# Performance work log

Hardware: AMD Instinct MI355X
Metric: run time of the kernel (lower is better)

The kernel has to match this reference:

```python
import jax, jax.numpy as jnp
import numpy as np
from math import factorial

N_SCALES = 4
K_ORI = 4
NA = 9


def _grids(h, w):
    fy = (jnp.arange(h) - h // 2) * (2.0 / h)
    fx = (jnp.arange(w) - w // 2) * (2.0 / w)
    FY, FX = jnp.meshgrid(fy, fx, indexing='ij')
    r = jnp.sqrt(FX ** 2 + FY ** 2)
    r = jnp.where(r == 0, 1.0 / max(h, w), r)
    return jnp.log2(r), jnp.arctan2(FY, FX)


def _rc_hi(lr, lo, hi):
    # sqrt raised-cosine rising 0->1 over log_rad in [lo, hi]
    t = jnp.clip((lr - lo) / (hi - lo), 0.0, 1.0)
    return jnp.sqrt(0.5 * (1.0 - jnp.cos(jnp.pi * t)))


def _rc_lo(lr, lo, hi):
    t = jnp.clip((lr - lo) / (hi - lo), 0.0, 1.0)
    return jnp.sqrt(0.5 * (1.0 + jnp.cos(jnp.pi * t)))


def _angle_masks(angle, K, is_complex):
    order = K - 1
    const = (2.0 ** (2 * order)) * (factorial(order) ** 2) / (K * factorial(2 * order))
    masks = []
    for b in range(K):
        d = jnp.mod(angle - jnp.pi * b / K + jnp.pi, 2 * jnp.pi) - jnp.pi
        if is_complex:  # single-sided (analytic) mask
            m = 2.0 * np.sqrt(const) * (jnp.cos(d) ** order) * (jnp.abs(d) < jnp.pi / 2)
        else:
            m = np.sqrt(const) * (jnp.cos(d) ** order)
        masks.append(m)
    return masks


def _build_pyramid(img, n_scales, K):
    # complex steerable pyramid in the frequency domain (tight_frame=False)
    order = K - 1
    h, w = img.shape
    imdft = jnp.fft.fftshift(jnp.fft.fft2(img))
    lr, ang = _grids(h, w)
    hi0 = _rc_hi(lr, -1.0, 0.0)
    lo0 = _rc_lo(lr, -1.0, 0.0)
    coeffs = {'residual_highpass': jnp.real(jnp.fft.ifft2(jnp.fft.ifftshift(imdft * hi0)))}
    lodft = imdft * lo0
    cph = (-1j) ** order
    for s in range(n_scales):
        hh, ww = lodft.shape
        lr, ang = _grids(hh, ww)
        him = _rc_hi(lr, -2.0, -1.0)
        for b, am in enumerate(_angle_masks(ang, K, True)):
            coeffs[(s, b)] = jnp.fft.ifft2(jnp.fft.ifftshift(cph * lodft * him * am))
        # spectral crop = spatial downsample by 2, then lowpass
        lodft = lodft[hh // 4: hh // 4 + hh // 2, ww // 4: ww // 4 + ww // 2]
        lr2, _ = _grids(hh // 2, ww // 2)
        lodft = lodft * _rc_lo(lr2, -1.0, 0.0)
    coeffs['residual_lowpass'] = jnp.real(jnp.fft.ifft2(jnp.fft.ifftshift(lodft)))
    return coeffs


def _lo0_filter(im):
    # height-0 pyramid residual lowpass == lo0 filtering (filterPyr in the torch code)
    h, w = im.shape
    lr, _ = _grids(h, w)
    return jnp.real(jnp.fft.ifft2(jnp.fft.ifftshift(jnp.fft.fftshift(jnp.fft.fft2(im)) * _rc_lo(lr, -1.0, 0.0))))


def _expand(im, f=2):
    # frequency-domain upsampling by factor f (Portilla_Simoncelli.expand)
    h, w = im.shape
    dft = jnp.fft.fftshift(jnp.fft.fft2(im)).astype(jnp.complex64)
    big = jnp.zeros((f * h, f * w), dtype=jnp.complex64)
    big = big.at[(f * h - h) // 2:(f * h - h) // 2 + h, (f * w - w) // 2:(f * w - w) // 2 + w].set(dft)
    return jnp.fft.ifft2(jnp.fft.ifftshift(big)) * (f * f)


def _recon_band(real_bands, K):
    # recon_pyr(levels=[0]) of a height-1 real pyramid whose bands were replaced
    order = K - 1
    h, w = real_bands[0].shape
    lr, ang = _grids(h, w)
    lo0 = _rc_lo(lr, -1.0, 0.0)
    him = _rc_hi(lr, -2.0, -1.0)
    ph = (1j) ** order
    recondft = jnp.zeros((h, w), dtype=jnp.complex64)
    for b, am in enumerate(_angle_masks(ang, K, False)):
        recondft = recondft + ph * jnp.fft.fftshift(jnp.fft.fft2(real_bands[b])) * him * am
    return jnp.real(jnp.fft.ifft2(jnp.fft.ifftshift(recondft * lo0)))


def _autocorr(ch, la):
    h, w = ch.shape
    F = jnp.fft.fft2(ch)
    ac = jnp.fft.fftshift(jnp.real(jnp.fft.ifft2(jnp.abs(F) ** 2))) / (h * w)
    cx, cy = h // 2, w // 2
    le = int(min(min(h, w) / 2 - 1, la))
    return ac[cx - le:cx + le + 1, cy - le:cy + le + 1], ac[cx, cy], le


def _skew_kurt(ch, vari, var0):
    cond = (vari / var0) > 1e-6
    skew = jnp.where(cond, jnp.mean(ch ** 3) / (vari ** 1.5), 0.0)
    kurt = jnp.where(cond, jnp.mean(ch ** 4) / (vari ** 2), 3.0)
    return skew, kurt


def _ps_forward(image):
    n_scales, K, Na = N_SCALES, K_ORI, NA
    img = image.reshape(image.shape[-2], image.shape[-1])
    mu = jnp.mean(img)
    var0 = jnp.var(img, ddof=1)
    cimg = img - mu
    pix = jnp.stack([mu, var0,
                     jnp.mean(cimg ** 3) / (var0 ** 1.5),
                     jnp.mean(cimg ** 4) / (var0 ** 2),
                     jnp.min(img), jnp.max(img)])
    coeffs = _build_pyramid(img, n_scales, K)
    coeffs['residual_lowpass'] = coeffs['residual_lowpass'] - jnp.mean(coeffs['residual_lowpass'])
    keys = ['residual_highpass'] + [(s, b) for s in range(n_scales) for b in range(K)] + ['residual_lowpass']
    mag, realc, mag_means = {}, {}, []
    for kk in keys:
        v = coeffs[kk]
        m = jnp.abs(v)
        mm = jnp.mean(m)
        mag_means.append(mm)
        mag[kk] = m - mm
        realc[kk] = jnp.real(v)
    mag_means = jnp.stack(mag_means)
    la = (Na - 1) // 2
    auto_corr = jnp.zeros((Na, Na, n_scales + 1))
    acm = jnp.zeros((Na, Na, n_scales, K))
    skew_r = jnp.zeros((n_scales + 1,))
    kurt_r = jnp.zeros((n_scales + 1,))
    recon = _lo0_filter(coeffs['residual_lowpass'])
    patch, vari, le = _autocorr(recon, la)
    auto_corr = auto_corr.at[la - le:la + le + 1, la - le:la + le + 1, n_scales].set(patch)
    sk, ku = _skew_kurt(recon, vari, var0)
    skew_r = skew_r.at[n_scales].set(sk)
    kurt_r = kurt_r.at[n_scales].set(ku)
    for s in range(n_scales - 1, -1, -1):
        for b in range(K):
            patch, vari, le = _autocorr(mag[(s, b)], la)
            acm = acm.at[la - le:la + le + 1, la - le:la + le + 1, s, b].set(patch)
        recon = jnp.real(_expand(recon, 2) / 4.0)
        recon = recon + _recon_band([realc[(s, b)] for b in range(K)], K)
        patch, vari, le = _autocorr(recon, la)
        auto_corr = auto_corr.at[la - le:la + le + 1, la - le:la + le + 1, s].set(patch)
        sk, ku = _skew_kurt(recon, vari, var0)
        skew_r = skew_r.at[s].set(sk)
        kurt_r = kurt_r.at[s].set(ku)
    K2 = max(2 * K, 5)
    coc_mag = jnp.zeros((K, K, n_scales + 1))
    csc_mag = jnp.zeros((K, K, n_scales))
    coc_real = jnp.zeros((K2, K2, n_scales + 1))
    csc_real = jnp.zeros((2 * K, K2, n_scales))
    for s in range(n_scales):
        hs, ws = realc[(s, 0)].shape
        csz = hs * ws
        if s < n_scales - 1:
            pars, rpr, rpi = [], [], []
            for b in range(K):
                tmp = _expand(coeffs[(s + 1, b)], 2) / 4.0
                rt, it = jnp.real(tmp), jnp.imag(tmp)
                mg = jnp.sqrt(rt ** 2 + it ** 2)
                a2 = 2.0 * jnp.arctan2(rt, it)  # note arg order matches torch code
                rpr.append((mg * jnp.cos(a2)).T.reshape(-1))
                rpi.append((mg * jnp.sin(a2)).T.reshape(-1))
                pars.append((mg - jnp.mean(mg)).T.reshape(-1))
            parents = jnp.stack(pars, 1)
            rparents = jnp.stack(rpr + rpi, 1)
        else:
            tmp = jnp.real(_expand(coeffs['residual_lowpass'], 2) / 4.0).T
            rparents = jnp.stack([tmp.reshape(-1),
                                  jnp.roll(tmp, 1, 0).reshape(-1),
                                  jnp.roll(tmp, -1, 0).reshape(-1),
                                  jnp.roll(tmp, 1, 1).reshape(-1),
                                  jnp.roll(tmp, -1, 1).reshape(-1)], 1)
            parents = None
        cousins = jnp.stack([mag[(s, b)].T.reshape(-1) for b in range(K)], 1)
        coc_mag = coc_mag.at[:, :, s].set(cousins.T @ cousins / csz)
        if parents is not None:
            csc_mag = csc_mag.at[:, :, s].set(cousins.T @ parents / csz)
        rcousins = jnp.stack([realc[(s, b)].T.reshape(-1) for b in range(K)], 1)
        coc_real = coc_real.at[:K, :K, s].set(rcousins.T @ rcousins / csz)
        nrp = rparents.shape[1]
        csc_real = csc_real.at[:K, :nrp, s].set(rcousins.T @ rparents / csz)
        if s == n_scales - 1:
            coc_real = coc_real.at[:nrp, :nrp, n_scales].set(rparents.T @ rparents / (csz / 4.0))
    var_hp = jnp.mean(coeffs['residual_highpass'] ** 2)
    return jnp.concatenate([pix, mag_means, acm.reshape(-1), skew_r, kurt_r,
                            auto_corr.reshape(-1), coc_mag.reshape(-1), csc_mag.reshape(-1),
                            coc_real.reshape(-1), csc_real.reshape(-1), var_hp.reshape(1)])


def setup_inputs() -> dict:
    key = jax.random.key(0)
    image = jax.random.normal(key, (1, 1, 1024, 1024), dtype=jnp.float32)
    return {"image": image}


def reference(image):
    return _ps_forward(image)
```

## Files before the change

### kernel.cpp

```cpp
#include <hip/hip_runtime.h>
#include <math.h>

typedef float2 cplx;

#define PI_F 3.14159265358979323846f
#define SQC  0.8944271909999159f

#define GS_FOR(i, n) for (int i = blockIdx.x * blockDim.x + threadIdx.x; i < (n); i += gridDim.x * blockDim.x)
#define RED_GRID 256

#define MD_PLAIN 0
#define MD_R2C   1
#define MD_HP    2
#define MD_BAND  3
#define MD_EMB   4

__device__ __forceinline__ float ufreq(int i, int n) {
  return (float)((i < (n >> 1)) ? i : i - n) * (2.0f / (float)n);
}
__device__ __forceinline__ void grid_lr_ang(int i, int j, int n, float* lr, float* ang) {
  float fy = ufreq(i, n), fx = ufreq(j, n);
  float r = sqrtf(fx * fx + fy * fy);
  if (i == 0 && j == 0) r = 1.0f / (float)n;
  *lr = log2f(r);
  *ang = atan2f(fy, fx);
}
__device__ __forceinline__ float rc_hi_f(float lr, float lo, float hi) {
  float t = (lr - lo) / (hi - lo);
  t = fminf(fmaxf(t, 0.0f), 1.0f);
  return sqrtf(0.5f * (1.0f - cosf(PI_F * t)));
}
__device__ __forceinline__ float rc_lo_f(float lr, float lo, float hi) {
  float t = (lr - lo) / (hi - lo);
  t = fminf(fmaxf(t, 0.0f), 1.0f);
  return sqrtf(0.5f * (1.0f + cosf(PI_F * t)));
}
__device__ __forceinline__ float wrap_d(float ang, int b) {
  float d = ang - PI_F * (float)b * 0.25f + PI_F;
  d = d - floorf(d * (0.5f / PI_F)) * (2.0f * PI_F);
  return d - PI_F;
}
__device__ __forceinline__ float amask_c(float ang, int b) {
  float d = wrap_d(ang, b);
  float c = cosf(d);
  float m = 2.0f * SQC * c * c * c;
  return (fabsf(d) < 0.5f * PI_F) ? m : 0.0f;
}
__device__ __forceinline__ float amask_r(float ang, int b) {
  float d = wrap_d(ang, b);
  float c = cosf(d);
  return SQC * c * c * c;
}

__device__ __forceinline__ double wred_d(double v) {
#pragma unroll
  for (int o = 32; o > 0; o >>= 1) v += __shfl_down(v, o);
  return v;
}
template<int NS>
__device__ __forceinline__ void block_to_parts(double* __restrict__ part, int slotBase, double* v) {
  __shared__ double lds[NS][4];
  const int wid = threadIdx.x >> 6, lane = threadIdx.x & 63;
#pragma unroll
  for (int q = 0; q < NS; ++q) {
    double r = wred_d(v[q]);
    if (lane == 0) lds[q][wid] = r;
  }
  __syncthreads();
  for (int q = threadIdx.x; q < NS; q += blockDim.x) {
    double s = lds[q][0] + lds[q][1] + lds[q][2] + lds[q][3];
    part[(size_t)(slotBase + q) * RED_GRID + blockIdx.x] = s;
  }
}
__global__ void reduce_parts_k(double* __restrict__ acc, const double* __restrict__ part, int base) {
  const double* p = part + (size_t)(base + blockIdx.x) * RED_GRID;
  double s = 0;
  for (int i = threadIdx.x; i < RED_GRID; i += 64) s += p[i];
  s = wred_d(s);
  if (threadIdx.x == 0) acc[base + blockIdx.x] = s;
}
__device__ __forceinline__ void atomicMinF(float* a, float v) {
  if (v >= 0.0f) atomicMin((int*)a, __float_as_int(v));
  else atomicMax((unsigned int*)a, __float_as_uint(v));
}
__device__ __forceinline__ void atomicMaxF(float* a, float v) {
  if (v >= 0.0f) atomicMax((int*)a, __float_as_int(v));
  else atomicMin((unsigned int*)a, __float_as_uint(v));
}

template<int LOGN, bool INV, int MODE>
__global__ __launch_bounds__(256) void fftm_k(cplx* __restrict__ dst, const void* __restrict__ srcv,
                                              const cplx* __restrict__ aux, int b0) {
  constexpr int N = 1 << LOGN;
  __shared__ cplx sh[N];
  __shared__ cplx tw[N / 2];
  const int tid = threadIdx.x;
  const int T = blockDim.x;
  const int r = blockIdx.x;
  const int i = r & (N - 1);
  const int p = r >> LOGN;
  for (int k = tid; k < N / 2; k += T) {
    float a = (INV ? 2.0f : -2.0f) * PI_F * (float)k / (float)N;
    float s, c;
    sincosf(a, &s, &c);
    tw[k] = make_float2(c, s);
  }
  for (int j = tid; j < N; j += T) {
    cplx v;
    if (MODE == MD_PLAIN) {
      v = ((const cplx*)srcv)[(size_t)r * N + j];
    } else if (MODE == MD_R2C) {
      v = make_float2(((const float*)srcv)[(size_t)r * N + j], 0.0f);
    } else if (MODE == MD_HP) {
      v = ((const cplx*)srcv)[(size_t)r * N + j];
      float lr, ang;
      grid_lr_ang(i, j, N, &lr, &ang);
      float h0 = rc_hi_f(lr, -1.0f, 0.0f);
      v.x *= h0; v.y *= h0;
    } else if (MODE == MD_BAND) {
      float lr, ang;
      grid_lr_ang(i, j, N, &lr, &ang);
      float m = rc_hi_f(lr, -2.0f, -1.0f) * amask_c(ang, b0 + p);
      cplx z = aux[i * N + j];
      v = make_float2(-z.y * m, z.x * m);
    } else {
      const int Nc = N >> 1, q = Nc >> 1;
      int ci = (i < q) ? i : ((i >= N - q) ? (i - N + Nc) : -1);
      int cj = (j < q) ? j : ((j >= N - q) ? (j - N + Nc) : -1);
      v = make_float2(0.0f, 0.0f);
      if (ci >= 0 && cj >= 0) {
        float lr, ang;
        grid_lr_ang(ci, cj, Nc, &lr, &ang);
        float m = rc_hi_f(lr, -2.0f, -1.0f) * amask_c(ang, b0 + p);
        cplx z = aux[ci * Nc + cj];
        v = make_float2(-z.y * m, z.x * m);
      }
    }
    unsigned rr = __brev((unsigned)j) >> (32 - LOGN);
    sh[rr] = v;
  }
  __syncthreads();
  for (int len = 2; len <= N; len <<= 1) {
    const int half = len >> 1;
    const int tstep = N / len;
    for (int j = tid; j < N / 2; j += T) {
      int pos = j & (half - 1);
      int base = (j - pos) << 1;
      cplx w = tw[pos * tstep];
      cplx a = sh[base + pos];
      cplx b = sh[base + pos + half];
      float tx = b.x * w.x - b.y * w.y;
      float ty = b.x * w.y + b.y * w.x;
      sh[base + pos] = make_float2(a.x + tx, a.y + ty);
      sh[base + pos + half] = make_float2(a.x - tx, a.y - ty);
    }
    __syncthreads();
  }
  const float sc = INV ? (1.0f / (float)N) : 1.0f;
  for (int j = tid; j < N; j += T) {
    cplx v = sh[j];
    dst[(size_t)r * N + j] = make_float2(v.x * sc, v.y * sc);
  }
}

__global__ void transpose_k(cplx* __restrict__ out, const cplx* __restrict__ in, int N) {
  __shared__ cplx tile[32][33];
  size_t po = (size_t)blockIdx.z * N * N;
  int bx = blockIdx.x * 32, by = blockIdx.y * 32;
  int x = bx + threadIdx.x;
  for (int dy = threadIdx.y; dy < 32; dy += 8)
    tile[dy][threadIdx.x] = in[po + (size_t)(by + dy) * N + x];
  __syncthreads();
  int xo = by + threadIdx.x;
  for (int dy = threadIdx.y; dy < 32; dy += 8)
    out[po + (size_t)(bx + dy) * N + xo] = tile[threadIdx.x][dy];
}

__global__ void lod_only_k(cplx* lod, const cplx* spec, int logN) {
  int N = 1 << logN, n = N * N;
  GS_FOR(idx, n) {
    int i = idx >> logN, j = idx & (N - 1);
    float lr, ang;
    grid_lr_ang(i, j, N, &lr, &ang);
    float l0 = rc_lo_f(lr, -1.0f, 0.0f);
    cplx z = spec[idx];
    lod[idx] = make_float2(z.x * l0, z.y * l0);
  }
}
__global__ void rhp_stats_k(const cplx* src, int n, double* part) {
  double sa = 0, sq = 0;
  GS_FOR(i, n) {
    float v = src[i].x;
    sa += fabsf(v);
    sq += (double)v * (double)v;
  }
  double v[2] = {sa, sq};
  block_to_parts<2>(part, 4, v);
}
template<int P>
__global__ void extract_band_k(float* realc, float* mag, const cplx* src, int logPer,
                               double* part, int slotBase) {
  int n = (1 << logPer) * P;
  double s0 = 0, s1 = 0, s2 = 0, s3 = 0;
  GS_FOR(idx, n) {
    cplx z = src[idx];
    float m = sqrtf(z.x * z.x + z.y * z.y);
    realc[idx] = z.x;
    mag[idx] = m;
    int p = idx >> logPer;
    if (p == 0) s0 += m; else if (p == 1) s1 += m; else if (p == 2) s2 += m; else s3 += m;
  }
  double v[4] = {s0, s1, s2, s3};
  block_to_parts<P>(part, slotBase, v);
}
__global__ void center_k(float* buf, int logPer, int P, const double* acc0) {
  int nPer = 1 << logPer, n = nPer * P;
  double inv = 1.0 / (double)nPer;
  GS_FOR(idx, n) buf[idx] -= (float)(acc0[idx >> logPer] * inv);
}
__global__ void lod_down_k(cplx* child, const cplx* par, int logNc) {
  int Nc = 1 << logNc, n = Nc * Nc, Np = Nc << 1;
  GS_FOR(idx, n) {
    int i = idx >> logNc, j = idx & (Nc - 1);
    int pi = (i < (Nc >> 1)) ? i : i + Nc;
    int pj = (j < (Nc >> 1)) ? j : j + Nc;
    float lr, ang;
    grid_lr_ang(i, j, Nc, &lr, &ang);
    float l0 = rc_lo_f(lr, -1.0f, 0.0f);
    cplx z = par[pi * Np + pj];
    child[idx] = make_float2(z.x * l0, z.y * l0);
  }
}
__global__ void sum_real2_k(const cplx* src, int n, double* part) {
  double s = 0;
  GS_FOR(i, n) s += (double)src[i].x;
  double v[1] = {s};
  block_to_parts<1>(part, 24, v);
}
__global__ void center_abs2_k(const cplx* src, int n, const double* acc, double* part) {
  float mu = (float)(acc[24] / (double)n);
  double s = 0;
  GS_FOR(i, n) s += fabsf(src[i].x - mu);
  double v[1] = {s};
  block_to_parts<1>(part, 25, v);
}
__global__ void rs4_init_k(cplx* rs, const cplx* lod4) {
  GS_FOR(idx, 4096) {
    int i = idx >> 6, j = idx & 63;
    float lr, ang;
    grid_lr_ang(i, j, 64, &lr, &ang);
    float l0 = rc_lo_f(lr, -1.0f, 0.0f);
    cplx v = lod4[idx];
    if (idx == 0) v = make_float2(0.0f, 0.0f);
    rs[idx] = make_float2(v.x * l0, v.y * l0);
  }
}
__global__ void embed_rs_k(cplx* dst, const cplx* src, int logNb, int zeroDC) {
  int Nb = 1 << logNb, Nc = Nb >> 1, q = Nc >> 1, n = Nb * Nb;
  GS_FOR(idx, n) {
    int i = idx >> logNb, j = idx & (Nb - 1);
    int ci = (i < q) ? i : ((i >= Nb - q) ? (i - Nb + Nc) : -1);
    int cj = (j < q) ? j : ((j >= Nb - q) ? (j - Nb + Nc) : -1);
    cplx v = make_float2(0.0f, 0.0f);
    if (ci >= 0 && cj >= 0) {
      v = src[ci * Nc + cj];
      if (zeroDC && ci == 0 && cj == 0) v = make_float2(0.0f, 0.0f);
    }
    dst[idx] = v;
  }
}
__global__ void recon_step_k(cplx* __restrict__ dst, const cplx* __restrict__ src,
                             const cplx* __restrict__ lod, int logNb) {
  int Nb = 1 << logNb, Nc = Nb >> 1, qq = Nc >> 1, n = Nb * Nb;
  GS_FOR(idx, n) {
    int i = idx >> logNb, j = idx & (Nb - 1);
    int ci = (i < qq) ? i : ((i >= Nb - qq) ? (i - Nb + Nc) : -1);
    int cj = (j < qq) ? j : ((j >= Nb - qq) ? (j - Nb + Nc) : -1);
    float ex = 0.0f, ey = 0.0f;
    if (ci >= 0 && cj >= 0) { cplx v = src[ci * Nc + cj]; ex = v.x; ey = v.y; }
    int ni = (Nb - i) & (Nb - 1), nj = (Nb - j) & (Nb - 1);
    float lr, ang;
    grid_lr_ang(i, j, Nb, &lr, &ang);
    float him = rc_hi_f(lr, -2.0f, -1.0f);
    float l0 = rc_lo_f(lr, -1.0f, 0.0f);
    cplx L = lod[idx];
    cplx L2 = lod[ni * Nb + nj];
    float sx = 0.0f, sy = 0.0f;
#pragma unroll
    for (int b = 0; b < 4; ++b) {
      float c1 = him * amask_c(ang, b);
      float c2 = him * amask_c(ang + PI_F, b);
      float mr = him * amask_r(ang, b);
      float gx = L.x * c1 - L2.x * c2;
      float gy = L.y * c1 + L2.y * c2;
      sx += 0.5f * mr * gx;
      sy += 0.5f * mr * gy;
    }
    dst[idx] = make_float2(ex + sx * l0, ey + sy * l0);
  }
}
template<int ST, bool SK>
__device__ __forceinline__ void ac_core(const float* __restrict__ xp, int logN,
                                        double* __restrict__ part, int slotBase) {
  const int N = 1 << logN;
  const int nu = (N * N) >> 3;
  float acc[41];
#pragma unroll
  for (int q = 0; q < 41; ++q) acc[q] = 0.0f;
  float a3 = 0.0f, a4 = 0.0f;
  for (int u = blockIdx.x * blockDim.x + threadIdx.x; u < nu; u += gridDim.x * blockDim.x) {
    int i = u >> (logN - 3);
    int j0 = (u & ((N >> 3) - 1)) << 3;
    float buf[5][16];
#pragma unroll
    for (int di = 0; di < 5; ++di) {
      int r = ((i + di) & (N - 1)) << logN;
#pragma unroll
      for (int blk = 0; blk < 4; ++blk) {
        int c = (j0 - 4 + blk * 4) & (N - 1);
        if (ST == 1) {
          const float4 v = *reinterpret_cast<const float4*>(xp + r + c);
          buf[di][blk * 4 + 0] = v.x; buf[di][blk * 4 + 1] = v.y;
          buf[di][blk * 4 + 2] = v.z; buf[di][blk * 4 + 3] = v.w;
        } else {
          const float4 v0 = *reinterpret_cast<const float4*>(xp + ((size_t)(r + c) << 1));
          const float4 v1 = *reinterpret_cast<const float4*>(xp + ((size_t)(r + c) << 1) + 4);
          buf[di][blk * 4 + 0] = v0.x; buf[di][blk * 4 + 1] = v0.z;
          buf[di][blk * 4 + 2] = v1.x; buf[di][blk * 4 + 3] = v1.z;
        }
      }
    }
#pragma unroll
    for (int k = 0; k < 8; ++k) {
      float xc = buf[0][4 + k];
      if (SK) {
        float x2 = xc * xc;
        a3 += x2 * xc;
        a4 += x2 * x2;
      }
#pragma unroll
      for (int q = 0; q < 41; ++q) {
        const int di = (q < 5) ? 0 : 1 + (q - 5) / 9;
        const int dj = (q < 5) ? q : ((q - 5) % 9) - 4;
        acc[q] += xc * buf[di][4 + k + dj];
      }
    }
  }
  constexpr int NS = SK ? 43 : 41;
  double v[NS];
#pragma unroll
  for (int q = 0; q < 41; ++q) v[q] = (double)acc[q];
  if (SK) { v[41] = (double)a3; v[42] = (double)a4; }
  block_to_parts<NS>(part, slotBase, v);
}
__global__ __launch_bounds__(256) void acm_vec_k(const float* m0, const float* m1,
                                                 const float* m2, const float* m3, double* part) {
  const int s = blockIdx.z;
  const float* base = (s == 0) ? m0 : ((s == 1) ? m1 : ((s == 2) ? m2 : m3));
  const int logN = 10 - s;
  const float* xp = base + ((size_t)blockIdx.y << (2 * logN));
  ac_core<1, false>(xp, logN, part, 448 + (s * 4 + blockIdx.y) * 41);
}
__global__ __launch_bounds__(256) void ac_rec_k(const float* x, int logN, double* part, int slotBase) {
  ac_core<2, true>(x, logN, part, slotBase);
}
__global__ void img_stats1_k(const float* img, int n, double* part, float* mm) {
  double s = 0;
  float mn = INFINITY, mx = -INFINITY;
  GS_FOR(i, n) {
    float v = img[i];
    s += (double)v;
    mn = fminf(mn, v);
    mx = fmaxf(mx, v);
  }
  double v[1] = {s};
  block_to_parts<1>(part, 0, v);
#pragma unroll
  for (int o = 32; o > 0; o >>= 1) {
    mn = fminf(mn, __shfl_down(mn, o));
    mx = fmaxf(mx, __shfl_down(mx, o));
  }
  if ((threadIdx.x & 63) == 0) {
    atomicMinF(mm + 0, mn);
    atomicMaxF(mm + 1, mx);
  }
}
__global__ void img_stats2_k(const float* img, int n, const double* acc, double* part) {
  double mu = acc[0] / (double)n;
  double s2 = 0, s3 = 0, s4 = 0;
  GS_FOR(i, n) {
    double c = (double)img[i] - mu;
    double c2 = c * c;
    s2 += c2;
    s3 += c2 * c;
    s4 += c2 * c2;
  }
  double v[3] = {s2, s3, s4};
  block_to_parts<3>(part, 1, v);
}
template<bool WS>
__global__ void gram4_k(const float* base, int n, double* part, int slotBase) {
  constexpr int NS = WS ? 20 : 16;
  double g[16];
  double s[4];
#pragma unroll
  for (int q = 0; q < 16; ++q) g[q] = 0;
#pragma unroll
  for (int q = 0; q < 4; ++q) s[q] = 0;
  GS_FOR(i, n) {
    double d0 = base[i], d1 = base[n + i], d2 = base[2 * n + i], d3 = base[3 * n + i];
    g[0] += d0 * d0; g[1] += d0 * d1; g[2]  += d0 * d2; g[3]  += d0 * d3;
    g[5] += d1 * d1; g[6] += d1 * d2; g[7]  += d1 * d3;
    g[10] += d2 * d2; g[11] += d2 * d3;
    g[15] += d3 * d3;
    if (WS) { s[0] += d0; s[1] += d1; s[2] += d2; s[3] += d3; }
  }
  g[4] = g[1]; g[8] = g[2]; g[12] = g[3]; g[9] = g[6]; g[13] = g[7]; g[14] = g[11];
  double v[NS];
#pragma unroll
  for (int q = 0; q < 16; ++q) v[q] = g[q];
  if (WS) {
#pragma unroll
    for (int q = 0; q < 4; ++q) v[16 + q] = s[q];
  }
  block_to_parts<NS>(part, slotBase, v);
}
__global__ void parent_reduce_k(const cplx* par, const float* magS, const float* realS, int n,
                                double* part, int slotBase) {
  double d[13];
#pragma unroll
  for (int q = 0; q < 13; ++q) d[q] = 0;
  GS_FOR(i, n) {
    cplx z = par[i];
    float rt = z.x, it = z.y;
    float mg = sqrtf(rt * rt + it * it);
    float rpr = 0.0f, rpi = 0.0f;
    if (mg > 0.0f) {
      rpr = (it * it - rt * rt) / mg;
      rpi = 2.0f * rt * it / mg;
    }
    d[0] += (double)mg;
#pragma unroll
    for (int b = 0; b < 4; ++b) d[1 + b] += (double)magS[b * n + i] * (double)mg;
#pragma unroll
    for (int b = 0; b < 4; ++b) {
      double rv = (double)realS[b * n + i];
      d[5 + b] += rv * (double)rpr;
      d[9 + b] += rv * (double)rpi;
    }
  }
  block_to_parts<13>(part, slotBase, d);
}
__global__ void lp_parent2_k(const cplx* X, const float* realS, int logN, double* part) {
  int N = 1 << logN, n = N * N;
  double d[45];
#pragma unroll
  for (int q = 0; q < 45; ++q) d[q] = 0;
  GS_FOR(idx, n) {
    int i = idx >> logN, j = idx & (N - 1);
    float c[5];
    c[0] = X[idx].x;
    c[1] = X[((i - 1) & (N - 1)) * N + j].x;
    c[2] = X[((i + 1) & (N - 1)) * N + j].x;
    c[3] = X[i * N + ((j - 1) & (N - 1))].x;
    c[4] = X[i * N + ((j + 1) & (N - 1))].x;
#pragma unroll
    for (int b = 0; b < 4; ++b) {
      double rv = (double)realS[b * n + idx];
#pragma unroll
      for (int k = 0; k < 5; ++k) d[b * 5 + k] += rv * (double)c[k];
    }
#pragma unroll
    for (int a = 0; a < 5; ++a)
#pragma unroll
      for (int k = 0; k < 5; ++k) d[20 + a * 5 + k] += (double)c[a] * (double)c[k];
  }
  block_to_parts<45>(part, 370, d);
}
__global__ void init_mm_k(float* mm) {
  if (threadIdx.x == 0) { mm[0] = INFINITY; mm[1] = -INFINITY; }
}

__global__ void assemble_k(float* out, const double* acc, const float* mm) {
  const int t = threadIdx.x;
  const double NPIX = 1048576.0;
  double var0 = acc[1] / (NPIX - 1.0);
  if (t == 0) {
    double mu = acc[0] / NPIX;
    out[0] = (float)mu;
    out[1] = (float)var0;
    out[2] = (float)((acc[2] / NPIX) / pow(var0, 1.5));
    out[3] = (float)((acc[3] / NPIX) / (var0 * var0));
    out[4] = mm[0];
    out[5] = mm[1];
    out[2455] = (float)(acc[5] / NPIX);
  }
  for (int k = t; k < 18; k += blockDim.x) {
    double n, sv;
    if (k == 0) { n = NPIX; sv = acc[4]; }
    else if (k == 17) { n = 4096.0; sv = acc[25]; }
    else { int s = (k - 1) >> 2; double dd = (double)(1024 >> s); n = dd * dd; sv = acc[7 + k]; }
    out[6 + k] = (float)(sv / n);
  }
  for (int si = t; si < 5; si += blockDim.x) {
    double dd = (si == 4) ? 64.0 : (double)(1024 >> si);
    double nn = dd * dd;
    double vari = acc[1104 + si * 43] / nn;
    bool cond = (vari / var0) > 1e-6;
    double m3 = acc[1104 + si * 43 + 41] / nn, m4 = acc[1104 + si * 43 + 42] / nn;
    out[1320 + si] = (float)(cond ? m3 / pow(vari, 1.5) : 0.0);
    out[1325 + si] = (float)(cond ? m4 / (vari * vari) : 3.0);
  }
  for (int w = t; w < 656; w += blockDim.x) {
    int patch = w / 41, q = w - patch * 41;
    int s = patch >> 2, b = patch & 3;
    double dd = (double)(1024 >> s);
    double v = acc[448 + w] / (dd * dd);
    int di = (q < 5) ? 0 : 1 + (q - 5) / 9;
    int dj = (q < 5) ? q : ((q - 5) % 9) - 4;
    int pi = 4 + dj, pj = 4 + di;
    out[24 + 144 * pi + 16 * pj + 4 * s + b] = (float)v;
    if (q) out[24 + 144 * (8 - pi) + 16 * (8 - pj) + 4 * s + b] = (float)v;
  }
  for (int w = t; w < 205; w += blockDim.x) {
    int si = w / 41, q = w - si * 41;
    double dd = (si == 4) ? 64.0 : (double)(1024 >> si);
    double v = acc[1104 + si * 43 + q] / (dd * dd);
    int di = (q < 5) ? 0 : 1 + (q - 5) / 9;
    int dj = (q < 5) ? q : ((q - 5) % 9) - 4;
    int pi = 4 + dj, pj = 4 + di;
    out[1330 + (pi * 9 + pj) * 5 + si] = (float)v;
    if (q) out[1330 + ((8 - pi) * 9 + (8 - pj)) * 5 + si] = (float)v;
  }
  for (int q = t; q < 64; q += blockDim.x) {
    int s = q >> 4, ij = q & 15;
    double dd = (double)(1024 >> s); double csz = dd * dd;
    out[1735 + ij * 5 + s] = (float)(acc[64 + s * 20 + ij] / csz);
  }
  for (int q = t; q < 64; q += blockDim.x) {
    int s = q >> 4, ij = q & 15;
    int i = ij >> 2, j = ij & 3;
    double dd = (double)(1024 >> s); double csz = dd * dd;
    out[1879 + (i * 8 + j) * 5 + s] = (float)(acc[144 + s * 16 + ij] / csz);
  }
  for (int q = t; q < 25; q += blockDim.x) {
    int a = q / 5, b2 = q - a * 5;
    out[1879 + (a * 8 + b2) * 5 + 4] = (float)(acc[390 + q] / 4096.0);
  }
  for (int q = t; q < 48; q += blockDim.x) {
    int s = q >> 4, ij = q & 15;
    int i = ij >> 2, pb = ij & 3;
    double dd = (double)(1024 >> s); double csz = dd * dd;
    const double* ps = acc + 208 + (s * 4 + pb) * 13;
    double meanp = ps[0] / csz;
    double cousSum = acc[64 + s * 20 + 16 + i];
    out[1815 + (i * 4 + pb) * 4 + s] = (float)((ps[1 + i] - meanp * cousSum) / csz);
  }
  for (int q = t; q < 96; q += blockDim.x) {
    int s = q >> 5, r = q & 31;
    int i = r >> 3, j = r & 7;
    int pb = j & 3, offq = (j >= 4) ? 9 : 5;
    double dd = (double)(1024 >> s); double csz = dd * dd;
    out[2199 + (i * 8 + j) * 4 + s] = (float)(acc[208 + (s * 4 + pb) * 13 + offq + i] / csz);
  }
  for (int q = t; q < 20; q += blockDim.x) {
    int i = q / 5, c = q - i * 5;
    out[2199 + (i * 8 + c) * 4 + 3] = (float)(acc[370 + q] / 16384.0);
  }
}

static inline int thr_for(int N) { return (N >= 512) ? 256 : ((N == 256) ? 128 : 64); }
template<int MODE>
static void fft_pass(int N, int rows, bool inv, cplx* dst, const void* src, const cplx* aux,
                     int b0, hipStream_t st) {
  dim3 g(rows), b(thr_for(N));
  switch (N) {
    case 64:
      if (inv) fftm_k<6, true, MODE><<<g, b, 0, st>>>(dst, src, aux, b0);
      else     fftm_k<6, false, MODE><<<g, b, 0, st>>>(dst, src, aux, b0);
      break;
    case 128:
      if (inv) fftm_k<7, true, MODE><<<g, b, 0, st>>>(dst, src, aux, b0);
      else     fftm_k<7, false, MODE><<<g, b, 0, st>>>(dst, src, aux, b0);
      break;
    case 256:
      if (inv) fftm_k<8, true, MODE><<<g, b, 0, st>>>(dst, src, aux, b0);
      else     fftm_k<8, false, MODE><<<g, b, 0, st>>>(dst, src, aux, b0);
      break;
    case 512:
      if (inv) fftm_k<9, true, MODE><<<g, b, 0, st>>>(dst, src, aux, b0);
      else     fftm_k<9, false, MODE><<<g, b, 0, st>>>(dst, src, aux, b0);
      break;
    case 1024:
      if (inv) fftm_k<10, true, MODE><<<g, b, 0, st>>>(dst, src, aux, b0);
      else     fftm_k<10, false, MODE><<<g, b, 0, st>>>(dst, src, aux, b0);
      break;
    default: break;
  }
}
static void transp(cplx* out, const cplx* in, int N, int P, hipStream_t st) {
  dim3 tg(N / 32, N / 32, P), tb(32, 8);
  transpose_k<<<tg, tb, 0, st>>>(out, in, N);
}
template<int MODE>
static void ifft2dT(int N, int P, cplx* out, cplx* tmp, const void* src, const cplx* aux,
                    int b0, hipStream_t st) {
  fft_pass<MODE>(N, N * P, true, tmp, src, aux, b0, st);
  transp(out, tmp, N, P, st);
  fft_pass<MD_PLAIN>(N, N * P, true, out, out, nullptr, 0, st);
}
static inline dim3 gsz(int n) {
  int b = (n + 255) >> 8;
  if (b > 2048) b = 2048;
  if (b < 1) b = 1;
  return dim3(b);
}

extern "C" void kernel_launch(void* const* d_in, const int* in_sizes, int n_in,
                              void* d_out, int out_size, void* d_ws, size_t ws_size,
                              hipStream_t stream) {
  (void)in_sizes; (void)n_in; (void)out_size; (void)ws_size;
  const float* img = (const float*)d_in[0];
  float* out = (float*)d_out;

  char* wsb = (char*)d_ws;
  size_t off = 0;
  auto alloc = [&](size_t bytes) -> void* {
    void* p = wsb + off;
    off += (bytes + 255) & ~(size_t)255;
    return p;
  };
  const size_t MB = (size_t)1 << 20;
  const int NSLOT = 1320;
  cplx* cA = (cplx*)alloc(16 * MB);
  cplx* cB = (cplx*)alloc(16 * MB);
  cplx* LOD[5];
  for (int s = 0; s < 5; ++s) {
    int N = 1024 >> s;
    LOD[s] = (cplx*)alloc((size_t)N * N * sizeof(cplx));
  }
  cplx* RS[4];
  for (int k = 0; k < 4; ++k) {
    int N = 64 << k;
    RS[k] = (cplx*)alloc((size_t)N * N * sizeof(cplx));
  }
  float* MAG[4];
  float* REALC[4];
  for (int s = 0; s < 4; ++s) {
    int N = 1024 >> s;
    MAG[s] = (float*)alloc((size_t)4 * N * N * sizeof(float));
  }
  for (int s = 0; s < 4; ++s) {
    int N = 1024 >> s;
    REALC[s] = (float*)alloc((size_t)4 * N * N * sizeof(float));
  }
  const int NPIX = 1024 * 1024;
  double* PART = (double*)alloc((size_t)NSLOT * RED_GRID * 8);
  double* ACC  = (double*)alloc(2048 * 8);
  float* MM    = (float*)alloc(256);

  auto finish = [&](int base, int count) {
    reduce_parts_k<<<dim3(count), 64, 0, stream>>>(ACC, PART, base);
  };

  hipMemsetAsync(out, 0, 2456 * sizeof(float), stream);
  init_mm_k<<<1, 64, 0, stream>>>(MM);

  img_stats1_k<<<dim3(RED_GRID), 256, 0, stream>>>(img, NPIX, PART, MM);
  finish(0, 1);
  img_stats2_k<<<dim3(RED_GRID), 256, 0, stream>>>(img, NPIX, ACC, PART);

  fft_pass<MD_R2C>(1024, 1024, false, cA, img, nullptr, 0, stream);
  transp(cB, cA, 1024, 1, stream);
  fft_pass<MD_PLAIN>(1024, 1024, false, cB, cB, nullptr, 0, stream);
  transp(cA, cB, 1024, 1, stream);
  lod_only_k<<<gsz(NPIX), 256, 0, stream>>>(LOD[0], cA, 10);
  ifft2dT<MD_HP>(1024, 1, cA, cB, cA, nullptr, 0, stream);
  rhp_stats_k<<<dim3(RED_GRID), 256, 0, stream>>>(cA, NPIX, PART);
  for (int b0 = 0; b0 < 4; b0 += 2) {
    ifft2dT<MD_BAND>(1024, 2, cB, cA, nullptr, LOD[0], b0, stream);
    extract_band_k<2><<<dim3(RED_GRID), 256, 0, stream>>>(REALC[0] + (size_t)b0 * NPIX,
                                                          MAG[0] + (size_t)b0 * NPIX, cB, 20, PART, 8 + b0);
  }
  finish(8, 4);
  center_k<<<gsz(4 * NPIX), 256, 0, stream>>>(MAG[0], 20, 4, ACC + 8);
  lod_down_k<<<gsz(512 * 512), 256, 0, stream>>>(LOD[1], LOD[0], 9);
  for (int s = 1; s <= 3; ++s) {
    int N = 1024 >> s, logN = 10 - s, n = N * N;
    ifft2dT<MD_BAND>(N, 4, cB, cA, nullptr, LOD[s], 0, stream);
    extract_band_k<4><<<dim3(RED_GRID), 256, 0, stream>>>(REALC[s], MAG[s], cB, 2 * logN, PART, 8 + 4 * s);
    finish(8 + 4 * s, 4);
    center_k<<<gsz(4 * n), 256, 0, stream>>>(MAG[s], 2 * logN, 4, ACC + 8 + 4 * s);
    lod_down_k<<<gsz((N / 2) * (N / 2)), 256, 0, stream>>>(LOD[s + 1], LOD[s], logN - 1);
  }
  ifft2dT<MD_PLAIN>(64, 1, cB, cA, LOD[4], nullptr, 0, stream);
  sum_real2_k<<<dim3(RED_GRID), 256, 0, stream>>>(cB, 4096, PART);
  finish(24, 1);
  center_abs2_k<<<dim3(RED_GRID), 256, 0, stream>>>(cB, 4096, ACC, PART);

  acm_vec_k<<<dim3(RED_GRID, 4, 4), 256, 0, stream>>>(MAG[0], MAG[1], MAG[2], MAG[3], PART);

  rs4_init_k<<<gsz(4096), 256, 0, stream>>>(RS[0], LOD[4]);
  ifft2dT<MD_PLAIN>(64, 1, cB, cA, RS[0], nullptr, 0, stream);
  ac_rec_k<<<dim3(RED_GRID), 256, 0, stream>>>((const float*)cB, 6, PART, 1104 + 4 * 43);
  cplx* cur = RS[0];
  for (int s = 3; s >= 0; --s) {
    int N = 1024 >> s, logN = 10 - s, n = N * N;
    cplx* sp = (s > 0) ? RS[4 - s] : cB;
    recon_step_k<<<gsz(n), 256, 0, stream>>>(sp, cur, LOD[s], logN);
    ifft2dT<MD_PLAIN>(N, 1, cB, cA, sp, nullptr, 0, stream);
    ac_rec_k<<<dim3(RED_GRID), 256, 0, stream>>>((const float*)cB, logN, PART, 1104 + s * 43);
    cur = sp;
  }

  for (int s = 0; s < 4; ++s) {
    int n = (1024 >> s) * (1024 >> s);
    gram4_k<true><<<dim3(RED_GRID), 256, 0, stream>>>(MAG[s], n, PART, 64 + s * 20);
    gram4_k<false><<<dim3(RED_GRID), 256, 0, stream>>>(REALC[s], n, PART, 144 + s * 16);
  }
  for (int pb0 = 0; pb0 < 4; pb0 += 2) {
    ifft2dT<MD_EMB>(1024, 2, cB, cA, nullptr, LOD[1], pb0, stream);
    for (int p = 0; p < 2; ++p)
      parent_reduce_k<<<dim3(RED_GRID), 256, 0, stream>>>(cB + (size_t)p * NPIX, MAG[0], REALC[0], NPIX,
                                                          PART, 208 + (pb0 + p) * 13);
  }
  for (int s = 1; s <= 2; ++s) {
    int N = 1024 >> s, n = N * N;
    ifft2dT<MD_EMB>(N, 4, cB, cA, nullptr, LOD[s + 1], 0, stream);
    for (int p = 0; p < 4; ++p)
      parent_reduce_k<<<dim3(RED_GRID), 256, 0, stream>>>(cB + (size_t)p * n, MAG[s], REALC[s], n,
                                                          PART, 208 + (s * 4 + p) * 13);
  }
  embed_rs_k<<<gsz(128 * 128), 256, 0, stream>>>(cA, LOD[4], 7, 1);
  ifft2dT<MD_PLAIN>(128, 1, cB, cA + 16384, cA, nullptr, 0, stream);
  lp_parent2_k<<<dim3(RED_GRID), 256, 0, stream>>>(cB, REALC[3], 7, PART);

  finish(0, NSLOT);
  assemble_k<<<1, 256, 0, stream>>>(out, ACC, MM);
}
```

Before: 1.152 ms.

## Replace centering passes with raw-moment corrections and batch reduction launches

Image statistics become a single pass that accumulates raw power sums; skew and kurtosis are then recovered algebraically in the final assembly. The per-scale centering kernels and their finish syncs are dropped, with the mean corrections applied in assembly for the magnitude autocorrelation and covariance. The eight gram launches are merged into one 2D-grid kernel, parent_reduce launches are batched over planes via blockIdx.y, and the reduction grid size is doubled. This cuts full-resolution passes, launches and serialising reductions. The cost is cancellation error from raw-moment formulas, and any consumer of the uncentered magnitudes that lacks a matching correction would produce wrong results.

```diff
diff --git a/kernel.cpp b/kernel.cpp
--- a/kernel.cpp
+++ b/kernel.cpp
@@ -7,7 +7,7 @@
 #define SQC  0.8944271909999159f
 
 #define GS_FOR(i, n) for (int i = blockIdx.x * blockDim.x + threadIdx.x; i < (n); i += gridDim.x * blockDim.x)
-#define RED_GRID 256
+#define RED_GRID 512
 
 #define MD_PLAIN 0
 #define MD_R2C   1
@@ -213,11 +213,6 @@
   double v[4] = {s0, s1, s2, s3};
   block_to_parts<P>(part, slotBase, v);
 }
-__global__ void center_k(float* buf, int logPer, int P, const double* acc0) {
-  int nPer = 1 << logPer, n = nPer * P;
-  double inv = 1.0 / (double)nPer;
-  GS_FOR(idx, n) buf[idx] -= (float)(acc0[idx >> logPer] * inv);
-}
 __global__ void lod_down_k(cplx* child, const cplx* par, int logNc) {
   int Nc = 1 << logNc, n = Nc * Nc, Np = Nc << 1;
   GS_FOR(idx, n) {
@@ -364,17 +359,18 @@
 __global__ __launch_bounds__(256) void ac_rec_k(const float* x, int logN, double* part, int slotBase) {
   ac_core<2, true>(x, logN, part, slotBase);
 }
-__global__ void img_stats1_k(const float* img, int n, double* part, float* mm) {
-  double s = 0;
+__global__ void img_stats_k(const float* img, int n, double* part, float* mm) {
+  double s1 = 0, s2 = 0, s3 = 0, s4 = 0;
   float mn = INFINITY, mx = -INFINITY;
   GS_FOR(i, n) {
-    float v = img[i];
-    s += (double)v;
-    mn = fminf(mn, v);
-    mx = fmaxf(mx, v);
-  }
-  double v[1] = {s};
-  block_to_parts<1>(part, 0, v);
+    float vf = img[i];
+    double v = (double)vf, v2 = v * v;
+    s1 += v; s2 += v2; s3 += v2 * v; s4 += v2 * v2;
+    mn = fminf(mn, vf);
+    mx = fmaxf(mx, vf);
+  }
+  double v[4] = {s1, s2, s3, s4};
+  block_to_parts<4>(part, 0, v);
 #pragma unroll
   for (int o = 32; o > 0; o >>= 1) {
     mn = fminf(mn, __shfl_down(mn, o));
@@ -385,48 +381,47 @@
     atomicMaxF(mm + 1, mx);
   }
 }
-__global__ void img_stats2_k(const float* img, int n, const double* acc, double* part) {
-  double mu = acc[0] / (double)n;
-  double s2 = 0, s3 = 0, s4 = 0;
-  GS_FOR(i, n) {
-    double c = (double)img[i] - mu;
-    double c2 = c * c;
-    s2 += c2;
-    s3 += c2 * c;
-    s4 += c2 * c2;
-  }
-  double v[3] = {s2, s3, s4};
-  block_to_parts<3>(part, 1, v);
-}
-template<bool WS>
-__global__ void gram4_k(const float* base, int n, double* part, int slotBase) {
-  constexpr int NS = WS ? 20 : 16;
+__global__ __launch_bounds__(256) void gram8_k(const float* m0, const float* m1, const float* m2,
+                                               const float* m3, const float* r0, const float* r1,
+                                               const float* r2, const float* r3, double* part) {
+  const int c = blockIdx.y;
+  const int s = c >> 1, isReal = c & 1;
+  const float* base = isReal ? ((s == 0) ? r0 : ((s == 1) ? r1 : ((s == 2) ? r2 : r3)))
+                             : ((s == 0) ? m0 : ((s == 1) ? m1 : ((s == 2) ? m2 : m3)));
+  const int n = (1024 >> s) * (1024 >> s);
   double g[16];
-  double s[4];
+  double ss[4];
 #pragma unroll
   for (int q = 0; q < 16; ++q) g[q] = 0;
 #pragma unroll
-  for (int q = 0; q < 4; ++q) s[q] = 0;
+  for (int q = 0; q < 4; ++q) ss[q] = 0;
   GS_FOR(i, n) {
     double d0 = base[i], d1 = base[n + i], d2 = base[2 * n + i], d3 = base[3 * n + i];
     g[0] += d0 * d0; g[1] += d0 * d1; g[2]  += d0 * d2; g[3]  += d0 * d3;
     g[5] += d1 * d1; g[6] += d1 * d2; g[7]  += d1 * d3;
     g[10] += d2 * d2; g[11] += d2 * d3;
     g[15] += d3 * d3;
-    if (WS) { s[0] += d0; s[1] += d1; s[2] += d2; s[3] += d3; }
+    if (!isReal) { ss[0] += d0; ss[1] += d1; ss[2] += d2; ss[3] += d3; }
   }
   g[4] = g[1]; g[8] = g[2]; g[12] = g[3]; g[9] = g[6]; g[13] = g[7]; g[14] = g[11];
-  double v[NS];
-#pragma unroll
-  for (int q = 0; q < 16; ++q) v[q] = g[q];
-  if (WS) {
-#pragma unroll
-    for (int q = 0; q < 4; ++q) v[16 + q] = s[q];
-  }
-  block_to_parts<NS>(part, slotBase, v);
-}
-__global__ void parent_reduce_k(const cplx* par, const float* magS, const float* realS, int n,
-                                double* part, int slotBase) {
+  if (isReal) {
+    double v[16];
+#pragma unroll
+    for (int q = 0; q < 16; ++q) v[q] = g[q];
+    block_to_parts<16>(part, 144 + s * 16, v);
+  } else {
+    double v[20];
+#pragma unroll
+    for (int q = 0; q < 16; ++q) v[q] = g[q];
+#pragma unroll
+    for (int q = 0; q < 4; ++q) v[16 + q] = ss[q];
+    block_to_parts<20>(part, 64 + s * 20, v);
+  }
+}
+__global__ void parent_reduce_k(const cplx* parBase, const float* magS, const float* realS, int n,
+                                double* part, int slotBase0) {
+  const int pl = blockIdx.y;
+  const cplx* par = parBase + (size_t)pl * n;
   double d[13];
 #pragma unroll
   for (int q = 0; q < 13; ++q) d[q] = 0;
@@ -449,7 +444,7 @@
       d[9 + b] += rv * (double)rpi;
     }
   }
-  block_to_parts<13>(part, slotBase, d);
+  block_to_parts<13>(part, slotBase0 + pl * 13, d);
 }
 __global__ void lp_parent2_k(const cplx* X, const float* realS, int logN, double* part) {
   int N = 1 << logN, n = N * N;
@@ -484,13 +479,16 @@
 __global__ void assemble_k(float* out, const double* acc, const float* mm) {
   const int t = threadIdx.x;
   const double NPIX = 1048576.0;
-  double var0 = acc[1] / (NPIX - 1.0);
+  const double muI = acc[0] / NPIX;
+  const double var0 = (acc[1] - NPIX * muI * muI) / (NPIX - 1.0);
   if (t == 0) {
-    double mu = acc[0] / NPIX;
-    out[0] = (float)mu;
+    out[0] = (float)muI;
     out[1] = (float)var0;
-    out[2] = (float)((acc[2] / NPIX) / pow(var0, 1.5));
-    out[3] = (float)((acc[3] / NPIX) / (var0 * var0));
+    double m3c = (acc[2] - 3.0 * muI * acc[1] + 2.0 * NPIX * muI * muI * muI) / NPIX;
+    double m4c = (acc[3] - 4.0 * muI * acc[2] + 6.0 * muI * muI * acc[1]
+                  - 3.0 * NPIX * muI * muI * muI * muI) / NPIX;
+    out[2] = (float)(m3c / pow(var0, 1.5));
+    out[3] = (float)(m4c / (var0 * var0));
     out[4] = mm[0];
     out[5] = mm[1];
     out[2455] = (float)(acc[5] / NPIX);
@@ -515,7 +513,9 @@
     int patch = w / 41, q = w - patch * 41;
     int s = patch >> 2, b = patch & 3;
     double dd = (double)(1024 >> s);
-    double v = acc[448 + w] / (dd * dd);
+    double nn = dd * dd;
+    double mb = acc[8 + s * 4 + b] / nn;
+    double v = acc[448 + w] / nn - mb * mb;
     int di = (q < 5) ? 0 : 1 + (q - 5) / 9;
     int dj = (q < 5) ? q : ((q - 5) % 9) - 4;
     int pi = 4 + dj, pj = 4 + di;
@@ -535,7 +535,9 @@
   for (int q = t; q < 64; q += blockDim.x) {
     int s = q >> 4, ij = q & 15;
     double dd = (double)(1024 >> s); double csz = dd * dd;
-    out[1735 + ij * 5 + s] = (float)(acc[64 + s * 20 + ij] / csz);
+    double mi = acc[8 + s * 4 + (ij >> 2)] / csz;
+    double mj = acc[8 + s * 4 + (ij & 3)] / csz;
+    out[1735 + ij * 5 + s] = (float)(acc[64 + s * 20 + ij] / csz - mi * mj);
   }
   for (int q = t; q < 64; q += blockDim.x) {
     int s = q >> 4, ij = q & 15;
@@ -666,9 +668,7 @@
   hipMemsetAsync(out, 0, 2456 * sizeof(float), stream);
   init_mm_k<<<1, 64, 0, stream>>>(MM);
 
-  img_stats1_k<<<dim3(RED_GRID), 256, 0, stream>>>(img, NPIX, PART, MM);
-  finish(0, 1);
-  img_stats2_k<<<dim3(RED_GRID), 256, 0, stream>>>(img, NPIX, ACC, PART);
+  img_stats_k<<<dim3(RED_GRID), 256, 0, stream>>>(img, NPIX, PART, MM);
 
   fft_pass<MD_R2C>(1024, 1024, false, cA, img, nullptr, 0, stream);
   transp(cB, cA, 1024, 1, stream);
@@ -682,15 +682,11 @@
     extract_band_k<2><<<dim3(RED_GRID), 256, 0, stream>>>(REALC[0] + (size_t)b0 * NPIX,
                                                           MAG[0] + (size_t)b0 * NPIX, cB, 20, PART, 8 + b0);
   }
-  finish(8, 4);
-  center_k<<<gsz(4 * NPIX), 256, 0, stream>>>(MAG[0], 20, 4, ACC + 8);
   lod_down_k<<<gsz(512 * 512), 256, 0, stream>>>(LOD[1], LOD[0], 9);
   for (int s = 1; s <= 3; ++s) {
-    int N = 1024 >> s, logN = 10 - s, n = N * N;
+    int N = 1024 >> s, logN = 10 - s;
     ifft2dT<MD_BAND>(N, 4, cB, cA, nullptr, LOD[s], 0, stream);
     extract_band_k<4><<<dim3(RED_GRID), 256, 0, stream>>>(REALC[s], MAG[s], cB, 2 * logN, PART, 8 + 4 * s);
-    finish(8 + 4 * s, 4);
-    center_k<<<gsz(4 * n), 256, 0, stream>>>(MAG[s], 2 * logN, 4, ACC + 8 + 4 * s);
     lod_down_k<<<gsz((N / 2) * (N / 2)), 256, 0, stream>>>(LOD[s + 1], LOD[s], logN - 1);
   }
   ifft2dT<MD_PLAIN>(64, 1, cB, cA, LOD[4], nullptr, 0, stream);
@@ -713,23 +709,18 @@
     cur = sp;
   }
 
-  for (int s = 0; s < 4; ++s) {
-    int n = (1024 >> s) * (1024 >> s);
-    gram4_k<true><<<dim3(RED_GRID), 256, 0, stream>>>(MAG[s], n, PART, 64 + s * 20);
-    gram4_k<false><<<dim3(RED_GRID), 256, 0, stream>>>(REALC[s], n, PART, 144 + s * 16);
-  }
+  gram8_k<<<dim3(RED_GRID, 8), 256, 0, stream>>>(MAG[0], MAG[1], MAG[2], MAG[3],
+                                                 REALC[0], REALC[1], REALC[2], REALC[3], PART);
   for (int pb0 = 0; pb0 < 4; pb0 += 2) {
     ifft2dT<MD_EMB>(1024, 2, cB, cA, nullptr, LOD[1], pb0, stream);
-    for (int p = 0; p < 2; ++p)
-      parent_reduce_k<<<dim3(RED_GRID), 256, 0, stream>>>(cB + (size_t)p * NPIX, MAG[0], REALC[0], NPIX,
-                                                          PART, 208 + (pb0 + p) * 13);
+    parent_reduce_k<<<dim3(RED_GRID, 2), 256, 0, stream>>>(cB, MAG[0], REALC[0], NPIX,
+                                                           PART, 208 + pb0 * 13);
   }
   for (int s = 1; s <= 2; ++s) {
     int N = 1024 >> s, n = N * N;
     ifft2dT<MD_EMB>(N, 4, cB, cA, nullptr, LOD[s + 1], 0, stream);
-    for (int p = 0; p < 4; ++p)
-      parent_reduce_k<<<dim3(RED_GRID), 256, 0, stream>>>(cB + (size_t)p * n, MAG[s], REALC[s], n,
-                                                          PART, 208 + (s * 4 + p) * 13);
+    parent_reduce_k<<<dim3(RED_GRID, 4), 256, 0, stream>>>(cB, MAG[s], REALC[s], n,
+                                                           PART, 208 + s * 4 * 13);
   }
   embed_rs_k<<<gsz(128 * 128), 256, 0, stream>>>(cA, LOD[4], 7, 1);
   ifft2dT<MD_PLAIN>(128, 1, cB, cA + 16384, cA, nullptr, 0, stream);
```

After: 1.069 ms. -7.2%, faster.
